# Performance work log

Measured on AMD Instinct MI355X. Metric: run time of the kernel, lower is better.

Reference implementation:

```python
import jax, jax.numpy as jnp
import numpy as np

KS = 3            # kernel_size
DILS = (1, 2, 4)  # dilation_list == padding_list
EPS = 1e-5        # BN eps


def _unfold3(x, d):
    # emulate F.unfold(kernel=3, dilation=d, padding=d, stride=1).view(b, c, 9, h, w)
    b, c, h, w = x.shape
    xp = jnp.pad(x, ((0, 0), (0, 0), (d, d), (d, d)))
    pats = [xp[:, :, i * d:i * d + h, j * d:j * d + w] for i in range(KS) for j in range(KS)]
    return jnp.stack(pats, axis=2)


def _conv1x1(x, w, b):
    return jnp.einsum('bchw,oc->bohw', x, w) + b[None, :, None, None]


def _bn_relu(x, g, be, m, v):
    s = g / jnp.sqrt(v + EPS)
    return jax.nn.relu(x * s[None, :, None, None] + (be - m * s)[None, :, None, None])


def _proj(x, w1, b1, g1, be1, m1, v1, w2, b2, g2, be2, m2, v2):
    h = _bn_relu(_conv1x1(x, w1, b1), g1, be1, m1, v1)
    return _bn_relu(_conv1x1(h, w2, b2), g2, be2, m2, v2)


def setup_inputs():
    key = jax.random.key(0)
    Cin, Ck, Cv, Cout = 512, 256, 256, 512
    B, H, W = 4, 64, 64
    ks = iter(jax.random.split(key, 48))

    def nrm(shape, s=0.02):
        return jax.random.normal(next(ks), shape, jnp.float32) * s

    def bn(c):
        return (jnp.ones((c,), jnp.float32) + nrm((c,), 0.1),  # gamma
                nrm((c,), 0.1),                                 # beta
                nrm((c,), 0.1),                                 # running mean
                jax.random.uniform(next(ks), (c,), jnp.float32, 0.5, 1.5))  # running var

    inp = {"x": jax.random.normal(next(ks), (B, Cin, H, W), jnp.float32)}
    for p in ("k", "q"):
        g1, be1, m1, v1 = bn(Ck)
        g2, be2, m2, v2 = bn(Ck)
        inp.update({
            p + "1_w": nrm((Ck, Cin)), p + "1_b": nrm((Ck,)),
            p + "1_g": g1, p + "1_be": be1, p + "1_m": m1, p + "1_v": v1,
            p + "2_w": nrm((Ck, Ck)), p + "2_b": nrm((Ck,)),
            p + "2_g": g2, p + "2_be": be2, p + "2_m": m2, p + "2_v": v2,
        })
    inp["v_w"] = nrm((Cv, Cin)); inp["v_b"] = nrm((Cv,))
    inp["w_w"] = nrm((Cout, Cv)); inp["w_b"] = nrm((Cout,))
    return inp


def reference(x,
              k1_w, k1_b, k1_g, k1_be, k1_m, k1_v,
              k2_w, k2_b, k2_g, k2_be, k2_m, k2_v,
              q1_w, q1_b, q1_g, q1_be, q1_m, q1_v,
              q2_w, q2_b, q2_g, q2_be, q2_m, q2_v,
              v_w, v_b, w_w, w_b):
    # scale == 1: MaxPool2d(1x1-equivalent) and final bilinear resize are identities.
    value = _conv1x1(x, v_w, v_b)                                  # (b,cv,h,w)
    keyf = _proj(x, k1_w, k1_b, k1_g, k1_be, k1_m, k1_v,
                 k2_w, k2_b, k2_g, k2_be, k2_m, k2_v)              # (b,ck,h,w)
    query = _proj(x, q1_w, q1_b, q1_g, q1_be, q1_m, q1_v,
                  q2_w, q2_b, q2_g, q2_be, q2_m, q2_v)             # (b,ck,h,w)
    uk = jnp.concatenate([_unfold3(keyf, d) for d in DILS], axis=2)   # (b,ck,27,h,w)
    uv = jnp.concatenate([_unfold3(value, d) for d in DILS], axis=2)  # (b,cv,27,h,w)
    sim = jnp.sum(uk * query[:, :, None], axis=1, keepdims=True)      # (b,1,27,h,w)
    sim = jax.nn.softmax(sim, axis=2)
    context = jnp.sum(sim * uv, axis=2)                               # (b,cv,h,w)
    return _conv1x1(context, w_w, w_b)
```

## Files before the change

### kernel.cpp

```cpp
#include <hip/hip_runtime.h>

#define HW   4096
#define Hh   64
#define Ww   64
#define NB   27
#define EPSBN 1e-5f

typedef _Float16 f16x8 __attribute__((ext_vector_type(8)));
typedef _Float16 f16x4 __attribute__((ext_vector_type(4)));
typedef _Float16 f16x2 __attribute__((ext_vector_type(2)));
typedef float    f32x4 __attribute__((ext_vector_type(4)));

__device__ __forceinline__ void gld_lds16(const void* g, void* l) {
    __builtin_amdgcn_global_load_lds(
        (const __attribute__((address_space(1))) unsigned int*)g,
        (__attribute__((address_space(3))) unsigned int*)l, 16, 0, 0);
}

__global__ __launch_bounds__(256)
void prep_kernel(const float* s0, const float* s1, const float* s2,
                 const float* s3, const float* s4, const float* s5,
                 _Float16* d0, _Float16* d1, _Float16* d2,
                 _Float16* d3, _Float16* d4, _Float16* d5)
{
    const int bid = blockIdx.x;
    const int j  = bid >> 6;
    const int bx = bid & 63;
    const float* s = j==0?s0: j==1?s1: j==2?s2: j==3?s3: j==4?s4: s5;
    _Float16*  d = j==0?d0: j==1?d1: j==2?d2: j==3?d3: j==4?d4: d5;
    const int  n = (j==3 || j==4) ? 65536 : 131072;
    const int  i = (bx * 256 + threadIdx.x) * 8;
    if (i < n) {
        f16x8 h;
        #pragma unroll
        for (int k = 0; k < 8; ++k) h[k] = (_Float16)s[i + k];
        *(f16x8*)(d + i) = h;
    }
}

struct GJob {
    const _Float16* in;
    const float*    xf;
    const _Float16* w;
    const float* b; const float* g; const float* be; const float* m; const float* v;
    _Float16* oh;
    float*    of;
};

__global__ __launch_bounds__(512, 2)
void gemm_f(GJob J0, GJob J1, GJob J2, int stage, int K, int JO, int mode)
{
    __shared__ _Float16 As[2][3][4096];
    __shared__ _Float16 Bs[2][16384];

    const int tid  = threadIdx.x;
    const int lane = tid & 63;
    const int w8   = tid >> 6;
    const int lr   = lane & 15;
    const int lg   = lane >> 4;
    const int wq   = w8 & 3;
    const int ph   = w8 >> 2;

    const int bid = blockIdx.x;
    const int xcd = bid & 7;
    const int jj  = bid >> 3;
    const int nb  = xcd * 8 + (jj >> 2);
    const int u   = jj & 3;

    const int nA = (stage == 1) ? 3 : 2;
    int js0, js1, js2, ob0, ob1, ob2;
    if (stage == 1)      { js0 = 0; js1 = 1; js2 = 2; ob0 = ob1 = ob2 = u * 64; }
    else if (stage == 2) { js0 = js1 = js2 = (u >> 1); ob0 = (u & 1) * 128; ob1 = ob0 + 64; ob2 = ob1; }
    else                 { js0 = js1 = js2 = 0; ob0 = u * 128; ob1 = ob0 + 64; ob2 = ob1; }

#define JSEL(js, f) ((js) == 0 ? J0.f : ((js) == 1 ? J1.f : J2.f))
    const _Float16* w0 = JSEL(js0, w);
    const _Float16* w1 = JSEL(js1, w);
    const _Float16* w2 = JSEL(js2, w);
    const float* b0 = JSEL(js0, b); const float* g0 = JSEL(js0, g);
    const float* be0 = JSEL(js0, be); const float* m0 = JSEL(js0, m); const float* v0 = JSEL(js0, v);
    const float* b1 = JSEL(js1, b); const float* g1 = JSEL(js1, g);
    const float* be1 = JSEL(js1, be); const float* m1 = JSEL(js1, m); const float* v1 = JSEL(js1, v);
    const float* b2 = JSEL(js2, b); const float* g2 = JSEL(js2, g);
    const float* be2 = JSEL(js2, be); const float* m2 = JSEL(js2, m); const float* v2 = JSEL(js2, v);
    _Float16* oh0 = JSEL(js0, oh); float* of0 = JSEL(js0, of);
    _Float16* oh1 = JSEL(js1, oh); float* of1 = JSEL(js1, of);
    _Float16* oh2 = JSEL(js2, oh); float* of2 = JSEL(js2, of);
    const _Float16* bIn = JSEL(js0, in);
    const float*    bXf = JSEL(js0, xf);
#undef JSEL

    const int scol = (((lane & 7) ^ (lane >> 3)) << 3);
    const int rowA = w8 * 8 + (lane >> 3);
    const _Float16* aS0 = w0 + (size_t)(ob0 + rowA) * K + scol;
    const _Float16* aS1 = w1 + (size_t)(ob1 + rowA) * K + scol;
    const _Float16* aS2 = w2 + (size_t)(ob2 + rowA) * K + scol;

    const int rowB = w8 * 32 + (lane >> 3);
    const _Float16* bS = bIn ? (bIn + (size_t)(nb * 256 + rowB) * K + scol) : nullptr;

    const int px   = tid & 255;
    const int chh  = tid >> 8;
    const int pgS  = nb * 256 + px;
    const float* xbase = bXf ? (bXf + (size_t)(pgS >> 12) * 512 * HW + (pgS & 4095)) : nullptr;
    const int bxk  = (px & 7) << 4;
    const bool f32B = (bXf != nullptr);

    float fr[32];
    auto ISSUE_BX = [&](int rd) {
        const int cb = rd * 64 + chh * 32;
        #pragma unroll
        for (int i2 = 0; i2 < 32; ++i2)
            fr[i2] = xbase[(size_t)(cb + i2) * HW];
    };
    auto WRITE_BX = [&](int buf) {
        #pragma unroll
        for (int g4 = 0; g4 < 4; ++g4) {
            f16x8 hv;
            #pragma unroll
            for (int i2 = 0; i2 < 8; ++i2) hv[i2] = (_Float16)fr[g4 * 8 + i2];
            *(f16x8*)((char*)&Bs[buf][0] + px * 128 + ((chh * 64 + g4 * 16) ^ bxk)) = hv;
        }
    };
    auto STAGE_B16 = [&](int buf, int rd) {
        const int kb = rd * 64;
        #pragma unroll
        for (int j2 = 0; j2 < 4; ++j2)
            gld_lds16(bS + (size_t)j2 * 8 * K + kb, (char*)&Bs[buf][0] + w8 * 4096 + j2 * 1024);
    };
    auto STAGE_A = [&](int buf, int rd) {
        const int kb = rd * 64;
        gld_lds16(aS0 + kb, (char*)&As[buf][0][0] + w8 * 1024);
        gld_lds16(aS1 + kb, (char*)&As[buf][1][0] + w8 * 1024);
        if (nA > 2) gld_lds16(aS2 + kb, (char*)&As[buf][2][0] + w8 * 1024);
    };

    f32x4 acc0[8] = {}, acc1[8] = {}, acc2[8] = {};
    const int nr = K >> 6;

    if (f32B) { ISSUE_BX(0); WRITE_BX(0); }
    else      { STAGE_B16(0, 0); }
    STAGE_A(0, 0);
    __syncthreads();

    int cur = 0;
    for (int rd = 0; rd < nr; ++rd) {
        const bool more = (rd + 1 < nr);
        if (more) {
            STAGE_A(cur ^ 1, rd + 1);
            if (f32B) ISSUE_BX(rd + 1);
            else      STAGE_B16(cur ^ 1, rd + 1);
        }

        #pragma unroll
        for (int ks = 0; ks < 2; ++ks) {
            const int colx = (ks * 64 + lg * 16) ^ ((lr & 7) << 4);
            f16x8 bfr[8];
            #pragma unroll
            for (int t = 0; t < 8; ++t)
                bfr[t] = *(const f16x8*)((const char*)&Bs[cur][0] + (ph * 128 + t * 16 + lr) * 128 + colx);
            const int aoff = (wq * 16 + lr) * 128 + colx;
            const f16x8 af0 = *(const f16x8*)((const char*)&As[cur][0][0] + aoff);
            const f16x8 af1 = *(const f16x8*)((const char*)&As[cur][1][0] + aoff);
            #pragma unroll
            for (int t = 0; t < 8; ++t)
                acc0[t] = __builtin_amdgcn_mfma_f32_16x16x32_f16(af0, bfr[t], acc0[t], 0, 0, 0);
            #pragma unroll
            for (int t = 0; t < 8; ++t)
                acc1[t] = __builtin_amdgcn_mfma_f32_16x16x32_f16(af1, bfr[t], acc1[t], 0, 0, 0);
            if (nA > 2) {
                const f16x8 af2 = *(const f16x8*)((const char*)&As[cur][2][0] + aoff);
                #pragma unroll
                for (int t = 0; t < 8; ++t)
                    acc2[t] = __builtin_amdgcn_mfma_f32_16x16x32_f16(af2, bfr[t], acc2[t], 0, 0, 0);
            }
        }

        if (f32B && more) WRITE_BX(cur ^ 1);
        __syncthreads();
        cur ^= 1;
    }

#define EPI(accS, obS, bS_, gS, beS, mS, vS, ohS, ofS) do {                      \
        const int o4 = (obS) + wq * 16 + lg * 4;                                 \
        float sc[4], off[4];                                                     \
        _Pragma("unroll")                                                        \
        for (int r = 0; r < 4; ++r) {                                            \
            const int o = o4 + r;                                                \
            if (gS) { float s = (gS)[o] * rsqrtf((vS)[o] + EPSBN);               \
                      sc[r] = s; off[r] = fmaf((bS_)[o] - (mS)[o], s, (beS)[o]); }\
            else    { sc[r] = 1.f; off[r] = (bS_)[o]; }                          \
        }                                                                        \
        _Pragma("unroll")                                                        \
        for (int t = 0; t < 8; ++t) {                                            \
            const int pg = nb * 256 + ph * 128 + t * 16 + lr;                    \
            float vv[4];                                                         \
            _Pragma("unroll")                                                    \
            for (int r = 0; r < 4; ++r) {                                        \
                float tv = fmaf(accS[t][r], sc[r], off[r]);                      \
                vv[r] = (gS) ? fmaxf(tv, 0.f) : tv;                              \
            }                                                                    \
            if (mode == 0) {                                                     \
                f16x4 hh;                                                        \
                _Pragma("unroll")                                                \
                for (int r = 0; r < 4; ++r) hh[r] = (_Float16)vv[r];             \
                *(f16x4*)((ohS) + (size_t)pg * JO + o4) = hh;                    \
            } else {                                                             \
                _Pragma("unroll")                                                \
                for (int r = 0; r < 4; ++r)                                      \
                    (ofS)[((size_t)(pg >> 12) * JO + o4 + r) * HW + (pg & 4095)] = vv[r]; \
            }                                                                    \
        }                                                                        \
    } while (0)

    EPI(acc0, ob0, b0, g0, be0, m0, v0, oh0, of0);
    EPI(acc1, ob1, b1, g1, be1, m1, v1, oh1, of1);
    if (nA > 2) EPI(acc2, ob2, b2, g2, be2, m2, v2, oh2, of2);
#undef EPI
}

__global__ __launch_bounds__(256)
void attn_fused(const _Float16* __restrict__ keyT, const _Float16* __restrict__ qryT,
                const _Float16* __restrict__ valT, _Float16* __restrict__ ctxT)
{
    const int tid  = threadIdx.x;
    const int slot = tid & 31;
    const int b    = blockIdx.y;
    const int p    = blockIdx.x * 8 + (tid >> 5);
    const int y    = p >> 6;
    const int xc   = p & 63;

    int   idx[NB];
    float valf[NB];
    #pragma unroll
    for (int n = 0; n < NB; ++n) {
        const int d  = (n < 9) ? 1 : (n < 18 ? 2 : 4);
        const int i  = (n / 3) % 3 - 1;
        const int j  = n % 3 - 1;
        const int yy = y + i * d, xx = xc + j * d;
        const bool ok = ((unsigned)yy < (unsigned)Hh) && ((unsigned)xx < (unsigned)Ww);
        idx[n]  = min(max(yy, 0), Hh - 1) * Ww + min(max(xx, 0), Ww - 1);
        valf[n] = ok ? 1.f : 0.f;
    }

    const size_t base = (size_t)b * HW * 256 + slot * 8;
    const f16x8 q8 = *(const f16x8*)(qryT + base + (size_t)p * 256);

    f16x2 qp[4];
    qp[0] = __builtin_shufflevector(q8, q8, 0, 1);
    qp[1] = __builtin_shufflevector(q8, q8, 2, 3);
    qp[2] = __builtin_shufflevector(q8, q8, 4, 5);
    qp[3] = __builtin_shufflevector(q8, q8, 6, 7);

    float sim[NB];
    #pragma unroll
    for (int n = 0; n < NB; ++n) {
        const f16x8 k8 = *(const f16x8*)(keyT + base + (size_t)idx[n] * 256);
        float s = 0.f;
        s = __builtin_amdgcn_fdot2(__builtin_shufflevector(k8, k8, 0, 1), qp[0], s, false);
        s = __builtin_amdgcn_fdot2(__builtin_shufflevector(k8, k8, 2, 3), qp[1], s, false);
        s = __builtin_amdgcn_fdot2(__builtin_shufflevector(k8, k8, 4, 5), qp[2], s, false);
        s = __builtin_amdgcn_fdot2(__builtin_shufflevector(k8, k8, 6, 7), qp[3], s, false);
        sim[n] = s;
    }

    #pragma unroll
    for (int n = 0; n < NB; ++n) {
        float s = sim[n];
        s += __shfl_xor(s, 1);
        s += __shfl_xor(s, 2);
        s += __shfl_xor(s, 4);
        s += __shfl_xor(s, 8);
        s += __shfl_xor(s, 16);
        sim[n] = s * valf[n];
    }

    float mx = sim[0];
    #pragma unroll
    for (int n = 1; n < NB; ++n) mx = fmaxf(mx, sim[n]);
    float sum = 0.f;
    #pragma unroll
    for (int n = 0; n < NB; ++n) { sim[n] = __expf(sim[n] - mx); sum += sim[n]; }
    const float inv = 1.f / sum;
    #pragma unroll
    for (int n = 0; n < NB; ++n) sim[n] = sim[n] * inv * valf[n];

    float acc[8];
    #pragma unroll
    for (int i = 0; i < 8; ++i) acc[i] = 0.f;
    #pragma unroll
    for (int n = 0; n < NB; ++n) {
        const f16x8 v8 = *(const f16x8*)(valT + base + (size_t)idx[n] * 256);
        const float w = sim[n];
        #pragma unroll
        for (int i = 0; i < 8; ++i) acc[i] = fmaf(w, (float)v8[i], acc[i]);
    }

    f16x8 h;
    #pragma unroll
    for (int i = 0; i < 8; ++i) h[i] = (_Float16)acc[i];
    *(f16x8*)(ctxT + base + (size_t)p * 256) = h;
}

extern "C" void kernel_launch(void* const* d_in, const int* in_sizes, int n_in,
                              void* d_out, int out_size, void* d_ws, size_t ws_size,
                              hipStream_t stream)
{
    (void)in_sizes; (void)n_in; (void)out_size; (void)ws_size;
    const float* x     = (const float*)d_in[0];
    const float* k1_w  = (const float*)d_in[1];
    const float* k1_b  = (const float*)d_in[2];
    const float* k1_g  = (const float*)d_in[3];
    const float* k1_be = (const float*)d_in[4];
    const float* k1_m  = (const float*)d_in[5];
    const float* k1_v  = (const float*)d_in[6];
    const float* k2_w  = (const float*)d_in[7];
    const float* k2_b  = (const float*)d_in[8];
    const float* k2_g  = (const float*)d_in[9];
    const float* k2_be = (const float*)d_in[10];
    const float* k2_m  = (const float*)d_in[11];
    const float* k2_v  = (const float*)d_in[12];
    const float* q1_w  = (const float*)d_in[13];
    const float* q1_b  = (const float*)d_in[14];
    const float* q1_g  = (const float*)d_in[15];
    const float* q1_be = (const float*)d_in[16];
    const float* q1_m  = (const float*)d_in[17];
    const float* q1_v  = (const float*)d_in[18];
    const float* q2_w  = (const float*)d_in[19];
    const float* q2_b  = (const float*)d_in[20];
    const float* q2_g  = (const float*)d_in[21];
    const float* q2_be = (const float*)d_in[22];
    const float* q2_m  = (const float*)d_in[23];
    const float* q2_v  = (const float*)d_in[24];
    const float* v_w   = (const float*)d_in[25];
    const float* v_b   = (const float*)d_in[26];
    const float* w_w   = (const float*)d_in[27];
    const float* w_b   = (const float*)d_in[28];

    _Float16* hw = (_Float16*)d_ws;
    const size_t SH = (size_t)4 * HW * 256;
    _Float16* wv_h  = hw;
    _Float16* wk1_h = wv_h  + 131072;
    _Float16* wq1_h = wk1_h + 131072;
    _Float16* wk2_h = wq1_h + 131072;
    _Float16* wq2_h = wk2_h + 65536;
    _Float16* ww_h  = wq2_h + 65536;
    _Float16* k1T   = ww_h  + 131072;
    _Float16* q1T   = k1T + SH;
    _Float16* valT  = q1T + SH;
    _Float16* ctxT  = valT + SH;
    _Float16* keyPC = ctxT + SH;
    _Float16* qryPC = keyPC + SH;

    prep_kernel<<<384, 256, 0, stream>>>(v_w, k1_w, q1_w, k2_w, q2_w, w_w,
                                         wv_h, wk1_h, wq1_h, wk2_h, wq2_h, ww_h);

    GJob jv  = { nullptr, x, wv_h,  v_b,  nullptr, nullptr, nullptr, nullptr, valT,  nullptr };
    GJob jk1 = { nullptr, x, wk1_h, k1_b, k1_g, k1_be, k1_m, k1_v,            k1T,   nullptr };
    GJob jq1 = { nullptr, x, wq1_h, q1_b, q1_g, q1_be, q1_m, q1_v,            q1T,   nullptr };
    GJob jk2 = { k1T, nullptr, wk2_h, k2_b, k2_g, k2_be, k2_m, k2_v,          keyPC, nullptr };
    GJob jq2 = { q1T, nullptr, wq2_h, q2_b, q2_g, q2_be, q2_m, q2_v,          qryPC, nullptr };
    GJob jw  = { ctxT, nullptr, ww_h, w_b,  nullptr, nullptr, nullptr, nullptr, nullptr, (float*)d_out };

    gemm_f<<<256, 512, 0, stream>>>(jv, jk1, jq1, 1, 512, 256, 0);
    gemm_f<<<256, 512, 0, stream>>>(jk2, jq2, jq2, 2, 256, 256, 0);
    attn_fused<<<dim3(512, 4), 256, 0, stream>>>(keyPC, qryPC, valT, ctxT);
    gemm_f<<<256, 512, 0, stream>>>(jw, jw, jw, 4, 256, 512, 2);
}
```

Measured before the change: 85.58 us.

## Merge all stages into one cooperative persistent kernel with grid syncs

Replaces the five separate launches (weight conversion, two projection GEMMs, attention, output GEMM) with a single cooperative kernel of 256 blocks. Stages are separated by grid-wide barriers, and the attention stage is remapped so each 512-thread block handles 64 pixels. This removes per-launch overhead and inter-kernel gaps. In exchange it adds grid-sync cost, and the attention phase now runs under the GEMM's 512-thread launch bounds and register budget, which may lower its occupancy.

```diff
diff --git a/kernel.cpp b/kernel.cpp
--- a/kernel.cpp
+++ b/kernel.cpp
@@ -1,4 +1,7 @@
 #include <hip/hip_runtime.h>
+#include <hip/hip_cooperative_groups.h>
+
+namespace cg = cooperative_groups;
 
 #define HW   4096
 #define Hh   64
@@ -15,27 +18,6 @@
     __builtin_amdgcn_global_load_lds(
         (const __attribute__((address_space(1))) unsigned int*)g,
         (__attribute__((address_space(3))) unsigned int*)l, 16, 0, 0);
-}
-
-__global__ __launch_bounds__(256)
-void prep_kernel(const float* s0, const float* s1, const float* s2,
-                 const float* s3, const float* s4, const float* s5,
-                 _Float16* d0, _Float16* d1, _Float16* d2,
-                 _Float16* d3, _Float16* d4, _Float16* d5)
-{
-    const int bid = blockIdx.x;
-    const int j  = bid >> 6;
-    const int bx = bid & 63;
-    const float* s = j==0?s0: j==1?s1: j==2?s2: j==3?s3: j==4?s4: s5;
-    _Float16*  d = j==0?d0: j==1?d1: j==2?d2: j==3?d3: j==4?d4: d5;
-    const int  n = (j==3 || j==4) ? 65536 : 131072;
-    const int  i = (bx * 256 + threadIdx.x) * 8;
-    if (i < n) {
-        f16x8 h;
-        #pragma unroll
-        for (int k = 0; k < 8; ++k) h[k] = (_Float16)s[i + k];
-        *(f16x8*)(d + i) = h;
-    }
 }
 
 struct GJob {
@@ -47,13 +29,21 @@
     float*    of;
 };
 
-__global__ __launch_bounds__(512, 2)
-void gemm_f(GJob J0, GJob J1, GJob J2, int stage, int K, int JO, int mode)
+struct MegaArgs {
+    const float* s0; const float* s1; const float* s2;
+    const float* s3; const float* s4; const float* s5;
+    _Float16* d0; _Float16* d1; _Float16* d2;
+    _Float16* d3; _Float16* d4; _Float16* d5;
+    GJob jv, jk1, jq1, jk2, jq2, jw;
+    const _Float16* keyPC; const _Float16* qryPC;
+    const _Float16* valT;  _Float16* ctxT;
+};
+
+__device__ __forceinline__ void gemm_phase(
+    _Float16* AsP, _Float16* BsP, int bid, int tid,
+    const GJob& J0, const GJob& J1, const GJob& J2,
+    int stage, int K, int JO, int mode)
 {
-    __shared__ _Float16 As[2][3][4096];
-    __shared__ _Float16 Bs[2][16384];
-
-    const int tid  = threadIdx.x;
     const int lane = tid & 63;
     const int w8   = tid >> 6;
     const int lr   = lane & 15;
@@ -61,7 +51,6 @@
     const int wq   = w8 & 3;
     const int ph   = w8 >> 2;
 
-    const int bid = blockIdx.x;
     const int xcd = bid & 7;
     const int jj  = bid >> 3;
     const int nb  = xcd * 8 + (jj >> 2);
@@ -90,6 +79,9 @@
     const float*    bXf = JSEL(js0, xf);
 #undef JSEL
 
+    char* Ab = (char*)AsP;
+    char* Bb = (char*)BsP;
+
     const int scol = (((lane & 7) ^ (lane >> 3)) << 3);
     const int rowA = w8 * 8 + (lane >> 3);
     const _Float16* aS0 = w0 + (size_t)(ob0 + rowA) * K + scol;
@@ -119,20 +111,20 @@
             f16x8 hv;
             #pragma unroll
             for (int i2 = 0; i2 < 8; ++i2) hv[i2] = (_Float16)fr[g4 * 8 + i2];
-            *(f16x8*)((char*)&Bs[buf][0] + px * 128 + ((chh * 64 + g4 * 16) ^ bxk)) = hv;
+            *(f16x8*)(Bb + buf * 32768 + px * 128 + ((chh * 64 + g4 * 16) ^ bxk)) = hv;
         }
     };
     auto STAGE_B16 = [&](int buf, int rd) {
         const int kb = rd * 64;
         #pragma unroll
         for (int j2 = 0; j2 < 4; ++j2)
-            gld_lds16(bS + (size_t)j2 * 8 * K + kb, (char*)&Bs[buf][0] + w8 * 4096 + j2 * 1024);
+            gld_lds16(bS + (size_t)j2 * 8 * K + kb, Bb + buf * 32768 + w8 * 4096 + j2 * 1024);
     };
     auto STAGE_A = [&](int buf, int rd) {
         const int kb = rd * 64;
-        gld_lds16(aS0 + kb, (char*)&As[buf][0][0] + w8 * 1024);
-        gld_lds16(aS1 + kb, (char*)&As[buf][1][0] + w8 * 1024);
-        if (nA > 2) gld_lds16(aS2 + kb, (char*)&As[buf][2][0] + w8 * 1024);
+        gld_lds16(aS0 + kb, Ab + buf * 24576 + w8 * 1024);
+        gld_lds16(aS1 + kb, Ab + buf * 24576 + 8192 + w8 * 1024);
+        if (nA > 2) gld_lds16(aS2 + kb, Ab + buf * 24576 + 16384 + w8 * 1024);
     };
 
     f32x4 acc0[8] = {}, acc1[8] = {}, acc2[8] = {};
@@ -158,10 +150,10 @@
             f16x8 bfr[8];
             #pragma unroll
             for (int t = 0; t < 8; ++t)
-                bfr[t] = *(const f16x8*)((const char*)&Bs[cur][0] + (ph * 128 + t * 16 + lr) * 128 + colx);
+                bfr[t] = *(const f16x8*)(Bb + cur * 32768 + (ph * 128 + t * 16 + lr) * 128 + colx);
             const int aoff = (wq * 16 + lr) * 128 + colx;
-            const f16x8 af0 = *(const f16x8*)((const char*)&As[cur][0][0] + aoff);
-            const f16x8 af1 = *(const f16x8*)((const char*)&As[cur][1][0] + aoff);
+            const f16x8 af0 = *(const f16x8*)(Ab + cur * 24576 + aoff);
+            const f16x8 af1 = *(const f16x8*)(Ab + cur * 24576 + 8192 + aoff);
             #pragma unroll
             for (int t = 0; t < 8; ++t)
                 acc0[t] = __builtin_amdgcn_mfma_f32_16x16x32_f16(af0, bfr[t], acc0[t], 0, 0, 0);
@@ -169,7 +161,7 @@
             for (int t = 0; t < 8; ++t)
                 acc1[t] = __builtin_amdgcn_mfma_f32_16x16x32_f16(af1, bfr[t], acc1[t], 0, 0, 0);
             if (nA > 2) {
-                const f16x8 af2 = *(const f16x8*)((const char*)&As[cur][2][0] + aoff);
+                const f16x8 af2 = *(const f16x8*)(Ab + cur * 24576 + 16384 + aoff);
                 #pragma unroll
                 for (int t = 0; t < 8; ++t)
                     acc2[t] = __builtin_amdgcn_mfma_f32_16x16x32_f16(af2, bfr[t], acc2[t], 0, 0, 0);
@@ -219,16 +211,15 @@
 #undef EPI
 }
 
-__global__ __launch_bounds__(256)
-void attn_fused(const _Float16* __restrict__ keyT, const _Float16* __restrict__ qryT,
-                const _Float16* __restrict__ valT, _Float16* __restrict__ ctxT)
+__device__ __forceinline__ void attn_phase(
+    const _Float16* __restrict__ keyT, const _Float16* __restrict__ qryT,
+    const _Float16* __restrict__ valT, _Float16* __restrict__ ctxT,
+    int P, int slot)
 {
-    const int tid  = threadIdx.x;
-    const int slot = tid & 31;
-    const int b    = blockIdx.y;
-    const int p    = blockIdx.x * 8 + (tid >> 5);
-    const int y    = p >> 6;
-    const int xc   = p & 63;
+    const int b  = P >> 12;
+    const int p  = P & 4095;
+    const int y  = p >> 6;
+    const int xc = p & 63;
 
     int   idx[NB];
     float valf[NB];
@@ -300,6 +291,58 @@
     #pragma unroll
     for (int i = 0; i < 8; ++i) h[i] = (_Float16)acc[i];
     *(f16x8*)(ctxT + base + (size_t)p * 256) = h;
+}
+
+__global__ __launch_bounds__(512, 2)
+void mega_kernel(MegaArgs a)
+{
+    __shared__ _Float16 As[2 * 3 * 4096];
+    __shared__ _Float16 Bs[2 * 16384];
+
+    cg::grid_group grid = cg::this_grid();
+    const int bid = blockIdx.x;
+    const int tid = threadIdx.x;
+    const int gtid = bid * 512 + tid;
+
+    auto CVT = [&](const float* s, _Float16* d, int n) {
+        const int i = gtid * 8;
+        if (i < n) {
+            f16x8 h;
+            #pragma unroll
+            for (int k = 0; k < 8; ++k) h[k] = (_Float16)s[i + k];
+            *(f16x8*)(d + i) = h;
+        }
+    };
+    CVT(a.s0, a.d0, 131072);
+    CVT(a.s1, a.d1, 131072);
+    CVT(a.s2, a.d2, 131072);
+    CVT(a.s3, a.d3, 65536);
+    CVT(a.s4, a.d4, 65536);
+    CVT(a.s5, a.d5, 131072);
+
+    grid.sync();
+
+    gemm_phase(As, Bs, bid, tid, a.jv, a.jk1, a.jq1, 1, 512, 256, 0);
+
+    grid.sync();
+
+    gemm_phase(As, Bs, bid, tid, a.jk2, a.jq2, a.jq2, 2, 256, 256, 0);
+
+    grid.sync();
+
+    {
+        const int slot = tid & 31;
+        const int pxo  = tid >> 5;
+        #pragma unroll
+        for (int it = 0; it < 4; ++it) {
+            const int P = (it * 256 + bid) * 16 + pxo;
+            attn_phase(a.keyPC, a.qryPC, a.valT, a.ctxT, P, slot);
+        }
+    }
+
+    grid.sync();
+
+    gemm_phase(As, Bs, bid, tid, a.jw, a.jw, a.jw, 4, 256, 512, 2);
 }
 
 extern "C" void kernel_launch(void* const* d_in, const int* in_sizes, int n_in,
@@ -352,18 +395,22 @@
     _Float16* keyPC = ctxT + SH;
     _Float16* qryPC = keyPC + SH;
 
-    prep_kernel<<<384, 256, 0, stream>>>(v_w, k1_w, q1_w, k2_w, q2_w, w_w,
-                                         wv_h, wk1_h, wq1_h, wk2_h, wq2_h, ww_h);
-
-    GJob jv  = { nullptr, x, wv_h,  v_b,  nullptr, nullptr, nullptr, nullptr, valT,  nullptr };
-    GJob jk1 = { nullptr, x, wk1_h, k1_b, k1_g, k1_be, k1_m, k1_v,            k1T,   nullptr };
-    GJob jq1 = { nullptr, x, wq1_h, q1_b, q1_g, q1_be, q1_m, q1_v,            q1T,   nullptr };
-    GJob jk2 = { k1T, nullptr, wk2_h, k2_b, k2_g, k2_be, k2_m, k2_v,          keyPC, nullptr };
-    GJob jq2 = { q1T, nullptr, wq2_h, q2_b, q2_g, q2_be, q2_m, q2_v,          qryPC, nullptr };
-    GJob jw  = { ctxT, nullptr, ww_h, w_b,  nullptr, nullptr, nullptr, nullptr, nullptr, (float*)d_out };
-
-    gemm_f<<<256, 512, 0, stream>>>(jv, jk1, jq1, 1, 512, 256, 0);
-    gemm_f<<<256, 512, 0, stream>>>(jk2, jq2, jq2, 2, 256, 256, 0);
-    attn_fused<<<dim3(512, 4), 256, 0, stream>>>(keyPC, qryPC, valT, ctxT);
-    gemm_f<<<256, 512, 0, stream>>>(jw, jw, jw, 4, 256, 512, 2);
+    MegaArgs ma;
+    ma.s0 = v_w;  ma.d0 = wv_h;
+    ma.s1 = k1_w; ma.d1 = wk1_h;
+    ma.s2 = q1_w; ma.d2 = wq1_h;
+    ma.s3 = k2_w; ma.d3 = wk2_h;
+    ma.s4 = q2_w; ma.d4 = wq2_h;
+    ma.s5 = w_w;  ma.d5 = ww_h;
+    ma.jv  = { nullptr, x, wv_h,  v_b,  nullptr, nullptr, nullptr, nullptr, valT,  nullptr };
+    ma.jk1 = { nullptr, x, wk1_h, k1_b, k1_g, k1_be, k1_m, k1_v,            k1T,   nullptr };
+    ma.jq1 = { nullptr, x, wq1_h, q1_b, q1_g, q1_be, q1_m, q1_v,            q1T,   nullptr };
+    ma.jk2 = { k1T, nullptr, wk2_h, k2_b, k2_g, k2_be, k2_m, k2_v,          keyPC, nullptr };
+    ma.jq2 = { q1T, nullptr, wq2_h, q2_b, q2_g, q2_be, q2_m, q2_v,          qryPC, nullptr };
+    ma.jw  = { ctxT, nullptr, ww_h, w_b,  nullptr, nullptr, nullptr, nullptr, nullptr, (float*)d_out };
+    ma.keyPC = keyPC; ma.qryPC = qryPC; ma.valT = valT; ma.ctxT = ctxT;
+
+    void* params[] = { (void*)&ma };
+    hipLaunchCooperativeKernel((const void*)mega_kernel, dim3(256), dim3(512),
+                               params, 0, stream);
 }
```

Result: slower. 204.3 us (+138.7%).
